# Kernel tuning notes

Measured on AMD Instinct MI355X. Metric: run time of the kernel, lower is better.

Reference implementation:

```python
import jax, jax.numpy as jnp
import numpy as np

S = 32          # input grid resolution
N = 2048        # active input voxels
C = 256         # in channels
CO = 128        # out channels
S2 = 2 * S      # upsampled resolution
M = 8 * N       # candidate child voxels
EPS = 1e-6


def setup_inputs() -> dict:
    key = jax.random.key(0)
    ks = jax.random.split(key, 8)
    # unique voxel coordinates (sparse occupancy)
    lin = jax.random.permutation(ks[0], S ** 3)[:N]
    coords = jnp.stack([lin // (S * S), (lin // S) % S, lin % S], axis=-1).astype(jnp.int32)
    sc = 0.05
    return {
        "feats": jax.random.normal(ks[1], (N, C), jnp.float32),
        "norm1_w": 1.0 + 0.1 * jax.random.normal(ks[2], (C,), jnp.float32),
        "norm1_b": 0.1 * jax.random.normal(ks[3], (C,), jnp.float32),
        "subdiv_w": sc * jax.random.normal(ks[4], (C, 8), jnp.float32),
        "subdiv_b": jnp.zeros((8,), jnp.float32),
        "conv1_w": sc * jax.random.normal(ks[5], (27, C, CO), jnp.float32),
        "conv1_b": jnp.zeros((CO,), jnp.float32),
        "conv2_w": sc * jax.random.normal(ks[6], (27, CO, CO), jnp.float32),
        "conv2_b": jnp.zeros((CO,), jnp.float32),
        "skip_w": sc * jax.random.normal(ks[7], (C, CO), jnp.float32),
        "skip_b": jnp.zeros((CO,), jnp.float32),
        "coords": coords,
    }


def _layernorm(x, w=None, b=None):
    # LayerNorm32: fp32 math, eps=1e-6
    m = jnp.mean(x, axis=-1, keepdims=True)
    v = jnp.var(x, axis=-1, keepdims=True)
    y = (x - m) * jax.lax.rsqrt(v + EPS)
    if w is not None:
        y = y * w + b
    return y


def _sparse_conv(feats, nidx, w, b):
    # submanifold 3x3x3 sparse conv: gather 27 neighbors, contract.
    # nidx: [M,27] with sentinel M pointing at a zero row.
    pad = jnp.concatenate([feats, jnp.zeros((1, feats.shape[1]), feats.dtype)], axis=0)
    g = pad[nidx]                                   # [M, 27, Cin]
    return jnp.einsum('nkc,kcd->nd', g, w) + b


def _forward(feats, norm1_w, norm1_b, subdiv_w, subdiv_b, conv1_w, conv1_b,
             conv2_w, conv2_b, skip_w, skip_b, coords):
    # subdiv prediction (SparseLinear C -> 8)
    subdiv = feats @ subdiv_w + subdiv_b            # [N, 8]
    # norm1 + silu
    h = jax.nn.silu(_layernorm(feats, norm1_w, norm1_b))
    # sparse upsample x2 with octree subdivision mask
    mask = (subdiv > 0).reshape(-1)                 # [M]
    j = jnp.arange(8, dtype=jnp.int32)
    offs8 = jnp.stack([(j >> 2) & 1, (j >> 1) & 1, j & 1], axis=-1)  # [8,3]
    cc = (coords[:, None, :] * 2 + offs8[None]).reshape(-1, 3)        # [M,3]
    h_c = jnp.where(mask[:, None], jnp.repeat(h, 8, axis=0), 0.0)     # [M,C]
    x_c = jnp.where(mask[:, None], jnp.repeat(feats, 8, axis=0), 0.0)
    # neighbor lookup grid (padded by 1; default M -> zero feature row)
    grid = jnp.full((S2 + 2, S2 + 2, S2 + 2), M, jnp.int32)
    grid = grid.at[cc[:, 0] + 1, cc[:, 1] + 1, cc[:, 2] + 1].set(
        jnp.arange(M, dtype=jnp.int32))
    d = jnp.arange(-1, 2, dtype=jnp.int32)
    offs27 = jnp.stack(jnp.meshgrid(d, d, d, indexing='ij'), axis=-1).reshape(27, 3)
    nc = cc[:, None, :] + 1 + offs27[None]          # [M,27,3]
    nidx = grid[nc[..., 0], nc[..., 1], nc[..., 2]] # [M,27]
    # conv1 -> norm2 (no affine) -> silu -> conv2
    h1 = jax.nn.silu(_layernorm(_sparse_conv(h_c, nidx, conv1_w, conv1_b)))
    h2 = _sparse_conv(h1, nidx, conv2_w, conv2_b)
    # residual with linear skip; mask out non-subdivided children
    out = (h2 + x_c @ skip_w + skip_b) * mask[:, None].astype(h2.dtype)
    return out, subdiv


def reference(feats, norm1_w, norm1_b, subdiv_w, subdiv_b, conv1_w, conv1_b,
              conv2_w, conv2_b, skip_w, skip_b, coords):
    return _forward(feats, norm1_w, norm1_b, subdiv_w, subdiv_b, conv1_w,
                    conv1_b, conv2_w, conv2_b, skip_w, skip_b, coords)
```

## Files before the change

### kernel.cpp

```cpp
#include <hip/hip_runtime.h>
#include <cstdint>
#include <cstddef>

constexpr int N  = 2048;
constexpr int C  = 256;
constexpr int CO = 128;
constexpr int M  = 16384;
constexpr int G  = 66;
constexpr int KP = 4;
constexpr int KCHUNK = 7;
constexpr float EPS = 1e-6f;

using bf8 = __attribute__((ext_vector_type(8))) short;
using f4  = __attribute__((ext_vector_type(4))) float;

static __device__ __forceinline__ unsigned short f2bf(float f) {
  unsigned u = __float_as_uint(f);
  u += 0x7fffu + ((u >> 16) & 1u);
  return (unsigned short)(u >> 16);
}
static __device__ __forceinline__ float bf2f(unsigned short s) {
  return __uint_as_float((unsigned)s << 16);
}

__global__ __launch_bounds__(256) void k_prep(
    const float* __restrict__ c1w, unsigned short* __restrict__ w1t,
    const float* __restrict__ c2w, unsigned short* __restrict__ w2t,
    int* __restrict__ grid, unsigned short* __restrict__ h,
    unsigned short* __restrict__ h1) {
  int i = blockIdx.x * 256 + threadIdx.x;
  if (i < G * G * G) grid[i] = M;
  if (blockIdx.x == 1200) {
    if (threadIdx.x < C) h[(size_t)N * C + threadIdx.x] = 0;
  }
  if (blockIdx.x == 1201) {
    if (threadIdx.x < CO) h1[(size_t)M * CO + threadIdx.x] = 0;
  }

  __shared__ float tile[32][33];
  int bx = blockIdx.x;
  const float* w; unsigned short* wtp; int cin, k, cb, ob;
  if (bx < 864) {
    w = c1w; wtp = w1t; cin = C;
    k = bx >> 5; int tl = bx & 31; cb = tl >> 2; ob = tl & 3;
  } else {
    int b2 = bx - 864;
    w = c2w; wtp = w2t; cin = CO;
    k = b2 >> 4; int tl = b2 & 15; cb = tl >> 2; ob = tl & 3;
  }
  int ty = threadIdx.x >> 5, tx = threadIdx.x & 31;
#pragma unroll
  for (int j = 0; j < 4; ++j) {
    int row = ty + j * 8;
    tile[row][tx] = w[((size_t)k * cin + cb * 32 + row) * CO + ob * 32 + tx];
  }
  __syncthreads();
#pragma unroll
  for (int j = 0; j < 4; ++j) {
    int row = ty + j * 8;
    wtp[((size_t)k * CO + ob * 32 + row) * cin + cb * 32 + tx] =
        f2bf(tile[tx][row]);
  }
}

__global__ __launch_bounds__(256) void k_rownorm(
    const float* __restrict__ feats, const float* __restrict__ n1w,
    const float* __restrict__ n1b, const float* __restrict__ sdw,
    const float* __restrict__ sdb, float* __restrict__ out_subdiv,
    unsigned short* __restrict__ h, int* __restrict__ pidx,
    float* __restrict__ maskf, const int* __restrict__ coords,
    int* __restrict__ grid) {
  int n = blockIdx.x, t = threadIdx.x;
  float x = feats[(size_t)n * C + t];
  float4 w0 = *(const float4*)(sdw + t * 8);
  float4 w1 = *(const float4*)(sdw + t * 8 + 4);
  float v[10] = {x * w0.x, x * w0.y, x * w0.z, x * w0.w,
                 x * w1.x, x * w1.y, x * w1.z, x * w1.w, x, x * x};
#pragma unroll
  for (int mk = 1; mk < 64; mk <<= 1) {
#pragma unroll
    for (int j = 0; j < 10; ++j) v[j] += __shfl_xor(v[j], mk, 64);
  }
  __shared__ float red[4][10];
  int wave = t >> 6, lane = t & 63;
  if (lane == 0) {
#pragma unroll
    for (int j = 0; j < 10; ++j) red[wave][j] = v[j];
  }
  __syncthreads();
  float sums[10];
#pragma unroll
  for (int j = 0; j < 10; ++j)
    sums[j] = red[0][j] + red[1][j] + red[2][j] + red[3][j];
  float mean = sums[8] / (float)C;
  float var  = sums[9] / (float)C - mean * mean;
  float rstd = rsqrtf(var + EPS);
  if (t < 8) {
    float sd = sums[t] + sdb[t];
    out_subdiv[(size_t)n * 8 + t] = sd;
    bool mk = sd > 0.f;
    pidx[n * 8 + t]  = mk ? n : N;
    maskf[n * 8 + t] = mk ? 1.f : 0.f;
    int xx = coords[n * 3 + 0] * 2 + ((t >> 2) & 1) + 1;
    int yy = coords[n * 3 + 1] * 2 + ((t >> 1) & 1) + 1;
    int zz = coords[n * 3 + 2] * 2 + (t & 1) + 1;
    grid[(xx * G + yy) * G + zz] = n * 8 + t;
  }
  float y  = (x - mean) * rstd * n1w[t] + n1b[t];
  float sl = y / (1.f + __expf(-y));
  h[(size_t)n * C + t] = f2bf(sl);
}

__global__ void k_nidx(const int* __restrict__ coords, const int* __restrict__ grid,
                       const int* __restrict__ pidx, int* __restrict__ nidxt,
                       int* __restrict__ g1t) {
  int idx = blockIdx.x * 256 + threadIdx.x;
  if (idx >= M * 27) return;
  int m = idx & (M - 1);
  int k = idx >> 14;
  int p = m >> 3, j = m & 7;
  int dx = k / 9 - 1;
  int dy = (k / 3) % 3 - 1;
  int dz = k % 3 - 1;
  int x = coords[p * 3 + 0] * 2 + ((j >> 2) & 1) + 1 + dx;
  int y = coords[p * 3 + 1] * 2 + ((j >> 1) & 1) + 1 + dy;
  int z = coords[p * 3 + 2] * 2 + (j & 1) + 1 + dz;
  int gv = grid[(x * G + y) * G + z];
  nidxt[idx] = gv;
  g1t[idx] = (gv == M) ? N : pidx[gv];
}

__global__ __launch_bounds__(256) void k_skip(const float* __restrict__ feats,
                                              const float* __restrict__ skw,
                                              const float* __restrict__ skb,
                                              float* __restrict__ s) {
  __shared__ float tile[32][36];
  int t = threadIdx.x;
  int rb = (blockIdx.x >> 1) * 32;
  int ob = (blockIdx.x & 1) * 64;
  int o = ob + (t & 63);
  int rg = (t >> 6) * 8;
  float acc[8] = {0, 0, 0, 0, 0, 0, 0, 0};
  for (int cb = 0; cb < C; cb += 32) {
    __syncthreads();
    int row = t >> 3, cc = (t & 7) * 4;
    *(float4*)&tile[row][cc] =
        *(const float4*)(feats + (size_t)(rb + row) * C + cb + cc);
    __syncthreads();
    for (int c = 0; c < 32; ++c) {
      float wv = skw[(size_t)(cb + c) * CO + o];
#pragma unroll
      for (int r = 0; r < 8; ++r) acc[r] += tile[rg + r][c] * wv;
    }
  }
  float bv = skb[o];
#pragma unroll
  for (int r = 0; r < 8; ++r) s[(size_t)(rb + rg + r) * CO + o] = acc[r] + bv;
}

template <int CIN, int NCB>
__global__ __launch_bounds__(256, 2) void k_conv(
    const unsigned short* __restrict__ src, const int* __restrict__ gt,
    const unsigned short* __restrict__ wt, unsigned short* __restrict__ part) {
  __shared__ unsigned short sB[2][128 * 32];
  const int t = threadIdx.x;
  const int w = t >> 6, lane = t & 63;
  const int quad = lane >> 4, ln = lane & 15;
  const int m0 = blockIdx.x * 128;
  const int kpart = blockIdx.y;
  const int k0 = kpart * KCHUNK;
  const int nk = min(KCHUNK, 27 - k0);
  const int nstage = nk * NCB;
  const int rh = (w >> 1) * 64, ch = (w & 1) * 64;

  const int row2 = t >> 1;
  const int c0 = (t & 1) * 2;
  const int x3 = (row2 >> 1) & 3;
  const int wsl0 = row2 * 32 + ((c0) ^ x3) * 8;
  const int wsl1 = row2 * 32 + ((c0 + 1) ^ x3) * 8;
  const int slot = (quad ^ ((ln >> 1) & 3)) * 8;

  const int* gbase = gt + (size_t)k0 * M + m0 + rh + ln;

  bf8 rb0, rb1;
  bf8 ra[4], rn[4];
  int ga[4], gn[4];

  auto loadB = [&](int s) {
    const int kk = s / NCB, cb = s - kk * NCB;
    const unsigned short* pb =
        wt + ((size_t)(k0 + kk) * CO + row2) * CIN + cb * 32 + c0 * 8;
    rb0 = *(const bf8*)(pb);
    rb1 = *(const bf8*)(pb + 8);
  };
  auto writeB = [&](int buf) {
    *(bf8*)(sB[buf] + wsl0) = rb0;
    *(bf8*)(sB[buf] + wsl1) = rb1;
  };

  f4 acc[16];
  f4 zero = {0.f, 0.f, 0.f, 0.f};
#pragma unroll
  for (int i = 0; i < 16; ++i) acc[i] = zero;

#pragma unroll
  for (int ti = 0; ti < 4; ++ti) ga[ti] = gbase[ti * 16];
  loadB(0);
#pragma unroll
  for (int ti = 0; ti < 4; ++ti)
    ra[ti] = *(const bf8*)(src + (size_t)ga[ti] * CIN + quad * 8);
  writeB(0);

  for (int s = 0; s < nstage; ++s) {
    const int buf = s & 1;
    const int kk = s / NCB, cb = s - kk * NCB;
    const bool have = (s + 1 < nstage);
    if (cb == 0 && kk + 1 < nk) {
#pragma unroll
      for (int ti = 0; ti < 4; ++ti) gn[ti] = gbase[(size_t)(kk + 1) * M + ti * 16];
    }
    if (have) {
      loadB(s + 1);
      const int cb1 = (cb + 1 < NCB) ? cb + 1 : 0;
      const int* gu = (cb + 1 < NCB) ? ga : gn;
#pragma unroll
      for (int ti = 0; ti < 4; ++ti)
        rn[ti] = *(const bf8*)(src + (size_t)gu[ti] * CIN + cb1 * 32 + quad * 8);
    }
    __syncthreads();
    const unsigned short* pb = sB[buf];
    bf8 bv[4];
#pragma unroll
    for (int tj = 0; tj < 4; ++tj)
      bv[tj] = *(const bf8*)(pb + (ch + tj * 16 + ln) * 32 + slot);
#pragma unroll
    for (int ti = 0; ti < 4; ++ti)
#pragma unroll
      for (int tj = 0; tj < 4; ++tj)
        acc[ti * 4 + tj] = __builtin_amdgcn_mfma_f32_16x16x32_bf16(
            ra[ti], bv[tj], acc[ti * 4 + tj], 0, 0, 0);
    if (have) {
      writeB(buf ^ 1);
#pragma unroll
      for (int ti = 0; ti < 4; ++ti) ra[ti] = rn[ti];
      if (cb + 1 == NCB) {
#pragma unroll
        for (int ti = 0; ti < 4; ++ti) ga[ti] = gn[ti];
      }
    }
  }

  unsigned short* pp = part + ((size_t)kpart * M + m0) * CO;
#pragma unroll
  for (int ti = 0; ti < 4; ++ti) {
    int mrow = rh + ti * 16 + quad * 4;
#pragma unroll
    for (int tj = 0; tj < 4; ++tj) {
      int co = ch + tj * 16 + ln;
#pragma unroll
      for (int rr = 0; rr < 4; ++rr)
        pp[(size_t)(mrow + rr) * CO + co] = f2bf(acc[ti * 4 + tj][rr]);
    }
  }
}

__global__ __launch_bounds__(256) void k_r1(const unsigned short* __restrict__ p,
                                            const float* __restrict__ bias,
                                            unsigned short* __restrict__ h1) {
  int wave = threadIdx.x >> 6, lane = threadIdx.x & 63;
  int m = blockIdx.x * 4 + wave;
  float v0 = bias[lane], v1 = bias[lane + 64];
#pragma unroll
  for (int q = 0; q < KP; ++q) {
    const unsigned short* pq = p + ((size_t)q * M + m) * CO;
    v0 += bf2f(pq[lane]);
    v1 += bf2f(pq[lane + 64]);
  }
  float sum = v0 + v1, sq = v0 * v0 + v1 * v1;
#pragma unroll
  for (int mk = 1; mk < 64; mk <<= 1) {
    sum += __shfl_xor(sum, mk, 64);
    sq  += __shfl_xor(sq, mk, 64);
  }
  float mean = sum / (float)CO;
  float var  = sq / (float)CO - mean * mean;
  float rstd = rsqrtf(var + EPS);
  float y0 = (v0 - mean) * rstd;
  float y1 = (v1 - mean) * rstd;
  float s0 = y0 / (1.f + __expf(-y0));
  float s1 = y1 / (1.f + __expf(-y1));
  h1[(size_t)m * CO + lane]      = f2bf(s0);
  h1[(size_t)m * CO + lane + 64] = f2bf(s1);
}

__global__ __launch_bounds__(256) void k_r2(const unsigned short* __restrict__ p,
                                            const float* __restrict__ bias,
                                            const float* __restrict__ sres,
                                            const float* __restrict__ maskf,
                                            float* __restrict__ out) {
  int i = blockIdx.x * 256 + threadIdx.x;
  int m = i >> 5;
  int o4 = (i & 31) * 4;
  float4 acc = *(const float4*)(bias + o4);
#pragma unroll
  for (int q = 0; q < KP; ++q) {
    ushort4 a = *(const ushort4*)(p + ((size_t)q * M + m) * CO + o4);
    acc.x += bf2f(a.x); acc.y += bf2f(a.y);
    acc.z += bf2f(a.z); acc.w += bf2f(a.w);
  }
  float4 s = *(const float4*)(sres + (size_t)(m >> 3) * CO + o4);
  float mk = maskf[m];
  float4 r;
  r.x = (acc.x + s.x) * mk;
  r.y = (acc.y + s.y) * mk;
  r.z = (acc.z + s.z) * mk;
  r.w = (acc.w + s.w) * mk;
  *(float4*)(out + (size_t)m * CO + o4) = r;
}

extern "C" void kernel_launch(void* const* d_in, const int* in_sizes, int n_in,
                              void* d_out, int out_size, void* d_ws, size_t ws_size,
                              hipStream_t stream) {
  const float* feats = (const float*)d_in[0];
  const float* n1w   = (const float*)d_in[1];
  const float* n1b   = (const float*)d_in[2];
  const float* sdw   = (const float*)d_in[3];
  const float* sdb   = (const float*)d_in[4];
  const float* c1w   = (const float*)d_in[5];
  const float* c1b   = (const float*)d_in[6];
  const float* c2w   = (const float*)d_in[7];
  const float* c2b   = (const float*)d_in[8];
  const float* skw   = (const float*)d_in[9];
  const float* skb   = (const float*)d_in[10];
  const int* coords  = (const int*)d_in[11];
  float* out = (float*)d_out;

  char* ws = (char*)d_ws;
  size_t off = 0;
  auto alloc = [&](size_t bytes) -> char* {
    char* p = ws + off;
    off += (bytes + 255) & ~(size_t)255;
    return p;
  };
  unsigned short* h    = (unsigned short*)alloc((size_t)(N + 1) * C * 2);
  unsigned short* h1   = (unsigned short*)alloc((size_t)(M + 1) * CO * 2);
  int*   grid  = (int*)alloc((size_t)G * G * G * 4);
  int*   nidxt = (int*)alloc((size_t)27 * M * 4);
  int*   g1t   = (int*)alloc((size_t)27 * M * 4);
  int*   pidx  = (int*)alloc((size_t)M * 4);
  float* maskf = (float*)alloc((size_t)M * 4);
  float* sres  = (float*)alloc((size_t)N * CO * 4);
  unsigned short* w1t = (unsigned short*)alloc((size_t)27 * CO * C * 2);
  unsigned short* w2t = (unsigned short*)alloc((size_t)27 * CO * CO * 2);
  unsigned short* pc  = (unsigned short*)alloc((size_t)KP * M * CO * 2);

  k_prep<<<1296, 256, 0, stream>>>(c1w, w1t, c2w, w2t, grid, h, h1);
  k_rownorm<<<N, 256, 0, stream>>>(feats, n1w, n1b, sdw, sdb,
                                   out + (size_t)M * CO, h, pidx, maskf,
                                   coords, grid);
  k_nidx<<<(M * 27 + 255) / 256, 256, 0, stream>>>(coords, grid, pidx, nidxt, g1t);
  k_skip<<<128, 256, 0, stream>>>(feats, skw, skb, sres);

  k_conv<C, 8><<<dim3(M / 128, KP), 256, 0, stream>>>(h, g1t, w1t, pc);
  k_r1<<<M / 4, 256, 0, stream>>>(pc, c1b, h1);

  k_conv<CO, 4><<<dim3(M / 128, KP), 256, 0, stream>>>(h1, nidxt, w2t, pc);
  k_r2<<<M * CO / 4 / 256, 256, 0, stream>>>(pc, c2b, sres, maskf, out);
}
```

Baseline: 198.4 us.

## Fuse skip linear into rownorm, split conv taps finer, raise conv occupancy

Removes the separate skip-GEMM kernel and computes the skip projection inside the per-row norm kernel, with each half of the threads reducing over half of the input channels through shared memory. The conv kernels now split the 27 taps into 7 partitions of 4 instead of 4 of 7, which doubles the number of blocks, and their launch bound rises to 4 blocks per CU. This is meant to remove a launch and improve parallelism and latency hiding in the convs. In exchange there are more partial buffers for the reduce kernels to sum, the 4-blocks-per-CU bound may force register spills, and each rownorm block now re-reads the full skip weight matrix.

```diff
diff --git a/kernel.cpp b/kernel.cpp
--- a/kernel.cpp
+++ b/kernel.cpp
@@ -7,8 +7,8 @@
 constexpr int CO = 128;
 constexpr int M  = 16384;
 constexpr int G  = 66;
-constexpr int KP = 4;
-constexpr int KCHUNK = 7;
+constexpr int KP = 7;
+constexpr int KCHUNK = 4;
 constexpr float EPS = 1e-6f;
 
 using bf8 = __attribute__((ext_vector_type(8))) short;
@@ -69,9 +69,13 @@
     const float* __restrict__ sdb, float* __restrict__ out_subdiv,
     unsigned short* __restrict__ h, int* __restrict__ pidx,
     float* __restrict__ maskf, const int* __restrict__ coords,
-    int* __restrict__ grid) {
+    int* __restrict__ grid, const float* __restrict__ skw,
+    const float* __restrict__ skb, float* __restrict__ sres) {
   int n = blockIdx.x, t = threadIdx.x;
+  __shared__ float sx[256];
+  __shared__ float sacc[256];
   float x = feats[(size_t)n * C + t];
+  sx[t] = x;
   float4 w0 = *(const float4*)(sdw + t * 8);
   float4 w1 = *(const float4*)(sdw + t * 8 + 4);
   float v[10] = {x * w0.x, x * w0.y, x * w0.z, x * w0.w,
@@ -109,6 +113,16 @@
   float y  = (x - mean) * rstd * n1w[t] + n1b[t];
   float sl = y / (1.f + __expf(-y));
   h[(size_t)n * C + t] = f2bf(sl);
+
+  int o = t & 127, half = t >> 7;
+  const float* wp = skw + (size_t)(half * 128) * CO + o;
+  const float* xs = sx + half * 128;
+  float a = 0.f;
+#pragma unroll 8
+  for (int c = 0; c < 128; ++c) a += xs[c] * wp[(size_t)c * CO];
+  sacc[t] = a;
+  __syncthreads();
+  if (t < 128) sres[(size_t)n * CO + t] = sacc[t] + sacc[t + 128] + skb[t];
 }
 
 __global__ void k_nidx(const int* __restrict__ coords, const int* __restrict__ grid,
@@ -130,36 +144,8 @@
   g1t[idx] = (gv == M) ? N : pidx[gv];
 }
 
-__global__ __launch_bounds__(256) void k_skip(const float* __restrict__ feats,
-                                              const float* __restrict__ skw,
-                                              const float* __restrict__ skb,
-                                              float* __restrict__ s) {
-  __shared__ float tile[32][36];
-  int t = threadIdx.x;
-  int rb = (blockIdx.x >> 1) * 32;
-  int ob = (blockIdx.x & 1) * 64;
-  int o = ob + (t & 63);
-  int rg = (t >> 6) * 8;
-  float acc[8] = {0, 0, 0, 0, 0, 0, 0, 0};
-  for (int cb = 0; cb < C; cb += 32) {
-    __syncthreads();
-    int row = t >> 3, cc = (t & 7) * 4;
-    *(float4*)&tile[row][cc] =
-        *(const float4*)(feats + (size_t)(rb + row) * C + cb + cc);
-    __syncthreads();
-    for (int c = 0; c < 32; ++c) {
-      float wv = skw[(size_t)(cb + c) * CO + o];
-#pragma unroll
-      for (int r = 0; r < 8; ++r) acc[r] += tile[rg + r][c] * wv;
-    }
-  }
-  float bv = skb[o];
-#pragma unroll
-  for (int r = 0; r < 8; ++r) s[(size_t)(rb + rg + r) * CO + o] = acc[r] + bv;
-}
-
 template <int CIN, int NCB>
-__global__ __launch_bounds__(256, 2) void k_conv(
+__global__ __launch_bounds__(256, 4) void k_conv(
     const unsigned short* __restrict__ src, const int* __restrict__ gt,
     const unsigned short* __restrict__ wt, unsigned short* __restrict__ part) {
   __shared__ unsigned short sB[2][128 * 32];
@@ -357,9 +343,8 @@
   k_prep<<<1296, 256, 0, stream>>>(c1w, w1t, c2w, w2t, grid, h, h1);
   k_rownorm<<<N, 256, 0, stream>>>(feats, n1w, n1b, sdw, sdb,
                                    out + (size_t)M * CO, h, pidx, maskf,
-                                   coords, grid);
+                                   coords, grid, skw, skb, sres);
   k_nidx<<<(M * 27 + 255) / 256, 256, 0, stream>>>(coords, grid, pidx, nidxt, g1t);
-  k_skip<<<128, 256, 0, stream>>>(feats, skw, skb, sres);
 
   k_conv<C, 8><<<dim3(M / 128, KP), 256, 0, stream>>>(h, g1t, w1t, pc);
   k_r1<<<M / 4, 256, 0, stream>>>(pc, c1b, h1);
```

After: 260.7 us. 1.31x slower.
